# Optimization experiments

Measured on AMD Instinct MI355X. Metric: run time of the kernel, lower is better.

The kernel has to match this reference:

```python
import jax, jax.numpy as jnp
import numpy as np

RES = 0.1
TABLE = 2 ** 20
MOD_T = 201
HEADS = 8
M = 500_000
D = 120
PRIMES_NP = np.array([73856093, 19349669, 83492791], dtype=np.int64)
BMIN = np.array([-2.6, -8.1, 0.0], dtype=np.float32)
BMAX = np.array([4.6, 4.7, 3.1], dtype=np.float32)
CORNERS = [(0, 0, 0), (1, 0, 0), (0, 1, 0), (0, 0, 1), (1, 1, 0), (1, 0, 1), (0, 1, 1), (1, 1, 1)]


def _build_hash_table():
    # Mirror torch.arange / meshgrid voxel grid construction.
    xs = np.arange(BMIN[0], BMAX[0], RES, dtype=np.float32)
    ys = np.arange(BMIN[1], BMAX[1], RES, dtype=np.float32)
    zs = np.arange(BMIN[2], BMAX[2], RES, dtype=np.float32)
    gx, gy, gz = np.meshgrid(xs, ys, zs, indexing='ij')
    vox = np.stack([gx, gy, gz], axis=-1).reshape(-1, 3)
    grid = np.floor(vox / RES).astype(np.int64)
    h = np.remainder((grid * PRIMES_NP).sum(-1), TABLE)
    buf = np.full(TABLE, -1, dtype=np.int64)
    uh, first_idx = np.unique(h, return_index=True)
    buf[uh] = first_idx
    return buf, vox.shape[0]


def setup_inputs() -> dict:
    key = jax.random.key(0)
    ks = jax.random.split(key, 12)
    buf_np, total_voxels = _build_hash_table()
    u = jax.random.uniform(ks[0], (M, 3), dtype=jnp.float32)
    query_pts = jnp.asarray(BMIN) + u * jnp.asarray(BMAX - BMIN)
    query_times = jax.random.randint(ks[1], (M,), 0, 1000, dtype=jnp.int64)
    dynamic_features = jax.random.normal(ks[2], (total_voxels, D), dtype=jnp.float32) * 0.01
    time_embeddings = jax.random.normal(ks[3], (MOD_T, D), dtype=jnp.float32) * 0.01
    s = 1.0 / np.sqrt(D)
    Wq = jax.random.normal(ks[4], (D, D), dtype=jnp.float32) * s
    Wk = jax.random.normal(ks[5], (D, D), dtype=jnp.float32) * s
    Wv = jax.random.normal(ks[6], (D, D), dtype=jnp.float32) * s
    Wo = jax.random.normal(ks[7], (D, D), dtype=jnp.float32) * s
    bq = jnp.zeros((D,), jnp.float32)
    bk = jnp.zeros((D,), jnp.float32)
    bv = jnp.zeros((D,), jnp.float32)
    bo = jnp.zeros((D,), jnp.float32)
    return {
        'query_pts': query_pts, 'query_times': query_times,
        'dynamic_features': dynamic_features, 'time_embeddings': time_embeddings,
        'buffer_voxel_index': jnp.asarray(buf_np),
        'Wq': Wq, 'bq': bq, 'Wk': Wk, 'bk': bk, 'Wv': Wv, 'bv': bv, 'Wo': Wo, 'bo': bo,
    }


def _attn_fuse(feat, time_emb, Wq, bq, Wk, bk, Wv, bv, Wo, bo):
    # 2-token self-attention fusion: tokens = [voxel feature, time embedding]
    m, d = feat.shape
    dh = d // HEADS
    x = jnp.stack([feat, time_emb], axis=1)  # (M, 2, D)
    q = (x @ Wq + bq).reshape(m, 2, HEADS, dh)
    k = (x @ Wk + bk).reshape(m, 2, HEADS, dh)
    v = (x @ Wv + bv).reshape(m, 2, HEADS, dh)
    scores = jnp.einsum('mqhd,mkhd->mhqk', q, k) / jnp.sqrt(jnp.float32(dh))
    a = jax.nn.softmax(scores, axis=-1)
    o = jnp.einsum('mhqk,mkhd->mqhd', a, v).reshape(m, 2, d)
    o = o @ Wo + bo
    return o.mean(axis=1)  # (M, D)


def reference(query_pts, query_times, dynamic_features, time_embeddings,
              buffer_voxel_index, Wq, bq, Wk, bk, Wv, bv, Wo, bo):
    primes = jnp.asarray(PRIMES_NP)
    m = query_pts.shape[0]
    d = dynamic_features.shape[1]
    t_mod = jnp.remainder(query_times, MOD_T)

    gf = query_pts / RES
    gfl = jnp.floor(gf)
    frac = gf - gfl                      # (M, 3)
    base = gfl.astype(jnp.int64)         # (M, 3)

    accum = jnp.zeros((m, d), dtype=query_pts.dtype)
    for ox, oy, oz in CORNERS:           # fixed structural 8-corner loop
        cc = base + jnp.asarray([ox, oy, oz], dtype=jnp.int64)
        h = jnp.remainder((cc * primes).sum(-1), TABLE)
        vidx = buffer_voxel_index[h]
        valid = vidx >= 0
        wx = frac[:, 0] if ox else 1.0 - frac[:, 0]
        wy = frac[:, 1] if oy else 1.0 - frac[:, 1]
        wz = frac[:, 2] if oz else 1.0 - frac[:, 2]
        w = wx * wy * wz                 # (M,)
        f = dynamic_features[jnp.where(valid, vidx, 0)]
        accum = accum + jnp.where(valid[:, None], f * w[:, None], 0.0)

    time_emb = time_embeddings[t_mod]
    return _attn_fuse(accum, time_emb, Wq, bq, Wk, bk, Wv, bv, Wo, bo)
```

## Files before the change

### kernel.cpp

```cpp
#include <hip/hip_runtime.h>
#include <math.h>

#define M_D   120
#define MOD_T 201
#define TABLE_MASK 0xFFFFFu
#define INV_S 0.25819888974716115f

#define WS_TV  1608
#define WS_TQK 27336

typedef float    f32x4 __attribute__((ext_vector_type(4)));
typedef uint32_t u32x4 __attribute__((ext_vector_type(4)));
typedef __fp16   f16x2v __attribute__((ext_vector_type(2)));
typedef __fp16   f16x8 __attribute__((ext_vector_type(8)));

union PK2 { f16x2v h; uint32_t u; };
union BFrag { f16x8 v; f16x2v h2[4]; uint32_t u[4]; };

__global__ void precomp_time(const float* __restrict__ temb,
                             const float* __restrict__ Wq, const float* __restrict__ bq,
                             const float* __restrict__ Wk, const float* __restrict__ bk,
                             const float* __restrict__ Wv, const float* __restrict__ bv,
                             float* __restrict__ ws) {
  const int t = blockIdx.x, np = threadIdx.x;
  const int h = np >> 4, m = np & 15;
  const bool valid = (m < 15);
  const int col = h * 15 + m;
  __shared__ float lq[128], lk[128];
  float q = 0.f, k = 0.f, v = 0.f;
  if (valid) {
    q = bq[col]; k = bk[col]; v = bv[col];
    const float* te = temb + t * M_D;
    for (int i = 0; i < M_D; ++i) {
      float x = te[i];
      q = fmaf(x, Wq[i * M_D + col], q);
      k = fmaf(x, Wk[i * M_D + col], k);
      v = fmaf(x, Wv[i * M_D + col], v);
    }
  }
  lq[np] = q; lk[np] = k;
  ws[WS_TV + t * 128 + np] = v;
  PK2 pk; pk.h[0] = (__fp16)(q * INV_S); pk.h[1] = (__fp16)k;
  ((uint32_t*)ws)[WS_TQK + t * 128 + np] = pk.u;
  __syncthreads();
  if (np < 8) {
    float s = 0.f;
    #pragma unroll
    for (int mm = 0; mm < 15; ++mm) s += lq[np * 16 + mm] * lk[np * 16 + mm];
    ws[t * 8 + np] = s * INV_S;
  }
}

__launch_bounds__(512, 2)
__global__ void fused_main(const float* __restrict__ qpts, const int* __restrict__ qtimes,
                           const float* __restrict__ dyn,  const int* __restrict__ hbuf,
                           const float* __restrict__ Wq, const float* __restrict__ bq,
                           const float* __restrict__ Wk, const float* __restrict__ bk,
                           const float* __restrict__ Wv, const float* __restrict__ bv,
                           const float* __restrict__ Wo, const float* __restrict__ bo,
                           const float* __restrict__ ws, float* __restrict__ out, int M) {
  __shared__ __align__(16) uint32_t wlds[4 * 8192];

  const int tid = threadIdx.x;
  for (int idx = tid; idx < 32768; idx += 512) {
    const int mat = idx >> 13, r = idx & 8191;
    const int nt = r >> 10, kk = (r >> 8) & 3, l = (r >> 2) & 63, d = r & 3;
    const int mm = l & 15;
    const int i0 = kk * 32 + ((l >> 4) << 3) + 2 * d;
    float v0 = 0.f, v1 = 0.f;
    if (mat < 3) {
      const float* W = (mat == 0) ? Wq : (mat == 1) ? Wk : Wv;
      const float* b = (mat == 0) ? bq : (mat == 1) ? bk : bv;
      if (mm < 15) {
        const int col = nt * 15 + mm;
        const int ia = i0, ib = i0 + 1;
        v0 = (ia < 120) ? W[ia * M_D + col] : (ia == 120 ? b[col] : 0.f);
        v1 = (ib < 120) ? W[ib * M_D + col] : (ib == 120 ? b[col] : 0.f);
        if (mat == 0) { v0 *= INV_S; v1 *= INV_S; }
      }
    } else {
      const int n = nt * 16 + mm;
      if (n < M_D) {
        #pragma unroll
        for (int e = 0; e < 2; ++e) {
          const int ip = i0 + e;
          const int hi = ip >> 4, mi = ip & 15;
          float vv = 0.f;
          if (mi < 15) vv = Wo[(hi * 15 + mi) * M_D + n];
          else if (ip == 15) vv = bo[n];
          if (e == 0) v0 = vv; else v1 = vv;
        }
      }
    }
    PK2 pk; pk.h[0] = (__fp16)v0; pk.h[1] = (__fp16)v1;
    wlds[idx] = pk.u;
  }
  __syncthreads();

  const int l = tid & 63, wv = tid >> 6;
  const int g = l >> 4, pl = l & 15, c0 = g << 2;
  const float* S11 = ws;
  const float* TVt = ws + WS_TV;
  const uint32_t* TQK = (const uint32_t*)ws + WS_TQK;

  const int T = (M + 15) >> 4;
  for (int tile = blockIdx.x * 8 + wv; tile < T; tile += gridDim.x * 8) {
    const int pid = (tile << 4) + pl;
    const int p = (pid < M) ? pid : (M - 1);

    const float px = qpts[3 * p], py = qpts[3 * p + 1], pz = qpts[3 * p + 2];
    const int tm = qtimes[p] % MOD_T;
    const float gx = px / 0.1f, gy = py / 0.1f, gz = pz / 0.1f;
    const float fx = floorf(gx), fy = floorf(gy), fz = floorf(gz);
    const float rx = gx - fx, ry = gy - fy, rz = gz - fz;
    const int bx = (int)fx, by = (int)fy, bz = (int)fz;

    f32x4 accA[4] = {{0,0,0,0},{0,0,0,0},{0,0,0,0},{0,0,0,0}};
    f32x4 accB[4] = {{0,0,0,0},{0,0,0,0},{0,0,0,0},{0,0,0,0}};
    const int i0g = g * 8;
    #pragma unroll
    for (int c = 0; c < 8; ++c) {
      const int ox = c & 1, oy = (c >> 1) & 1, oz = c >> 2;
      const uint32_t hh = (uint32_t)(bx + ox) * 73856093u +
                          (uint32_t)(by + oy) * 19349669u +
                          (uint32_t)(bz + oz) * 83492791u;
      const int vc = hbuf[hh & TABLE_MASK];
      const float wc = (ox ? rx : 1.f - rx) * (oy ? ry : 1.f - ry) * (oz ? rz : 1.f - rz);
      if (vc >= 0) {
        const float* fr = dyn + (long)vc * M_D + i0g;
        #pragma unroll
        for (int kk = 0; kk < 4; ++kk) {
          if (kk < 3 || g < 3) {
            f32x4 lo4 = *(const f32x4*)(fr + kk * 32);
            f32x4 hi4 = *(const f32x4*)(fr + kk * 32 + 4);
            accA[kk] += lo4 * wc;
            accB[kk] += hi4 * wc;
          }
        }
      }
    }
    if (g == 3) accA[3][0] = 1.0f;

    BFrag bf[4];
    #pragma unroll
    for (int kk = 0; kk < 4; ++kk) {
      bf[kk].h2[0] = __builtin_amdgcn_cvt_pkrtz(accA[kk][0], accA[kk][1]);
      bf[kk].h2[1] = __builtin_amdgcn_cvt_pkrtz(accA[kk][2], accA[kk][3]);
      bf[kk].h2[2] = __builtin_amdgcn_cvt_pkrtz(accB[kk][0], accB[kk][1]);
      bf[kk].h2[3] = __builtin_amdgcn_cvt_pkrtz(accB[kk][2], accB[kk][3]);
    }

    f32x4 tvv[8]; u32x4 tqk[8]; float s11v[8];
    #pragma unroll
    for (int nt = 0; nt < 8; ++nt) {
      tvv[nt] = *(const f32x4*)(TVt + tm * 128 + nt * 16 + c0);
      tqk[nt] = *(const u32x4*)(TQK + tm * 128 + nt * 16 + c0);
      s11v[nt] = S11[tm * 8 + nt];
    }

    f32x4 aq[8], ak[8], av[8];
    #pragma unroll
    for (int nt = 0; nt < 8; ++nt) {
      f32x4 zq = {0,0,0,0}, zk = {0,0,0,0}, zv = {0,0,0,0};
      #pragma unroll
      for (int kk = 0; kk < 4; ++kk) {
        const int off = nt * 1024 + kk * 256 + l * 4;
        f16x8 a0 = *(const f16x8*)(wlds + off);
        f16x8 a1 = *(const f16x8*)(wlds + 8192 + off);
        f16x8 a2 = *(const f16x8*)(wlds + 16384 + off);
        zq = __builtin_amdgcn_mfma_f32_16x16x32_f16(a0, bf[kk].v, zq, 0, 0, 0);
        zk = __builtin_amdgcn_mfma_f32_16x16x32_f16(a1, bf[kk].v, zk, 0, 0, 0);
        zv = __builtin_amdgcn_mfma_f32_16x16x32_f16(a2, bf[kk].v, zv, 0, 0, 0);
      }
      aq[nt] = zq; ak[nt] = zk; av[nt] = zv;
    }

    float a_[8], b_[8];
    #pragma unroll
    for (int nt = 0; nt < 8; ++nt) {
      float s00 = 0.f, s01 = 0.f, s10 = 0.f;
      #pragma unroll
      for (int r = 0; r < 4; ++r) {
        const float qv = aq[nt][r], kv = ak[nt][r];
        PK2 tt; tt.u = tqk[nt][r];
        const float tqs = (float)tt.h[0], tk = (float)tt.h[1];
        s00 = fmaf(qv, kv, s00);
        s01 = fmaf(qv, tk, s01);
        s10 = fmaf(tqs, kv, s10);
      }
      s00 += __shfl_xor(s00, 16); s00 += __shfl_xor(s00, 32);
      s01 += __shfl_xor(s01, 16); s01 += __shfl_xor(s01, 32);
      s10 += __shfl_xor(s10, 16); s10 += __shfl_xor(s10, 32);
      const float s11 = s11v[nt];
      const float m0 = fmaxf(s00, s01), m1 = fmaxf(s10, s11);
      const float e00 = __expf(s00 - m0), e01 = __expf(s01 - m0);
      const float e10 = __expf(s10 - m1), e11 = __expf(s11 - m1);
      const float r0 = 1.f / (e00 + e01), r1 = 1.f / (e10 + e11);
      a_[nt] = 0.5f * (e00 * r0 + e10 * r1);
      b_[nt] = 0.5f * (e01 * r0 + e11 * r1);
    }

    uint32_t cdw[8][2];
    #pragma unroll
    for (int nt = 0; nt < 8; ++nt) {
      f32x4 cv;
      #pragma unroll
      for (int r = 0; r < 4; ++r) cv[r] = a_[nt] * av[nt][r] + b_[nt] * tvv[nt][r];
      if (nt == 0 && g == 3) cv[3] = 1.0f;
      PK2 p0, p1;
      p0.h = __builtin_amdgcn_cvt_pkrtz(cv[0], cv[1]);
      p1.h = __builtin_amdgcn_cvt_pkrtz(cv[2], cv[3]);
      cdw[nt][0] = p0.u; cdw[nt][1] = p1.u;
    }

    const int src0 = pl | ((g & 1) << 5);
    const int src1 = src0 + 16;
    const bool hsel = (g >= 2);
    BFrag bco[4];
    #pragma unroll
    for (int kk = 0; kk < 4; ++kk) {
      #pragma unroll
      for (int d = 0; d < 4; ++d) {
        const int s = (d >= 2) ? src1 : src0;
        const int vlo = __shfl((int)cdw[2 * kk][d & 1], s, 64);
        const int vhi = __shfl((int)cdw[2 * kk + 1][d & 1], s, 64);
        bco[kk].u[d] = hsel ? (uint32_t)vhi : (uint32_t)vlo;
      }
    }

    float* orow = out + (long)pid * M_D;
    #pragma unroll
    for (int nt = 0; nt < 8; ++nt) {
      f32x4 zo = {0,0,0,0};
      #pragma unroll
      for (int kk = 0; kk < 4; ++kk) {
        f16x8 a3 = *(const f16x8*)(wlds + 24576 + nt * 1024 + kk * 256 + l * 4);
        zo = __builtin_amdgcn_mfma_f32_16x16x32_f16(a3, bco[kk].v, zo, 0, 0, 0);
      }
      if (pid < M && (nt < 7 || g < 2))
        *(f32x4*)(orow + nt * 16 + c0) = zo;
    }
  }
}

extern "C" void kernel_launch(void* const* d_in, const int* in_sizes, int n_in,
                              void* d_out, int out_size, void* d_ws, size_t ws_size,
                              hipStream_t stream) {
  const float* qpts   = (const float*)d_in[0];
  const int*   qtimes = (const int*)d_in[1];
  const float* dyn    = (const float*)d_in[2];
  const float* temb   = (const float*)d_in[3];
  const int*   hbuf   = (const int*)d_in[4];
  const float* Wq = (const float*)d_in[5];
  const float* bq = (const float*)d_in[6];
  const float* Wk = (const float*)d_in[7];
  const float* bk = (const float*)d_in[8];
  const float* Wv = (const float*)d_in[9];
  const float* bv = (const float*)d_in[10];
  const float* Wo = (const float*)d_in[11];
  const float* bo = (const float*)d_in[12];
  float* out = (float*)d_out;
  float* ws  = (float*)d_ws;
  const int M = in_sizes[1];

  hipLaunchKernelGGL(precomp_time, dim3(MOD_T), dim3(128), 0, stream,
                     temb, Wq, bq, Wk, bk, Wv, bv, ws);
  hipLaunchKernelGGL(fused_main, dim3(256), dim3(512), 0, stream,
                     qpts, qtimes, dyn, hbuf, Wq, bq, Wk, bk, Wv, bv, Wo, bo, ws, out, M);
}
```

Measured before the change: 1.119 ms.

## Use 1024-thread blocks and make corner gathers branchless with kk-outer accumulation

Doubles the block size to 1024 threads (16 waves per block, one block per CU), so the 128 KB LDS weight copy is shared by twice as many waves and fewer blocks redo the LDS fill. The eight-corner gather is restructured: hash lookups first produce per-corner pointers and weights, with invalid corners redirected to row 0 at weight zero. The accumulation loop is then reordered so the k-slice is outermost, which needs only one pair of accumulators at a time and gives branchless loads the compiler can batch. The risks are higher register pressure under the 1024-thread launch bound and extra loads for invalid corners.

```diff
diff --git a/kernel.cpp b/kernel.cpp
--- a/kernel.cpp
+++ b/kernel.cpp
@@ -51,7 +51,7 @@
   }
 }
 
-__launch_bounds__(512, 2)
+__launch_bounds__(1024, 1)
 __global__ void fused_main(const float* __restrict__ qpts, const int* __restrict__ qtimes,
                            const float* __restrict__ dyn,  const int* __restrict__ hbuf,
                            const float* __restrict__ Wq, const float* __restrict__ bq,
@@ -62,7 +62,7 @@
   __shared__ __align__(16) uint32_t wlds[4 * 8192];
 
   const int tid = threadIdx.x;
-  for (int idx = tid; idx < 32768; idx += 512) {
+  for (int idx = tid; idx < 32768; idx += 1024) {
     const int mat = idx >> 13, r = idx & 8191;
     const int nt = r >> 10, kk = (r >> 8) & 3, l = (r >> 2) & 63, d = r & 3;
     const int mm = l & 15;
@@ -104,7 +104,7 @@
   const uint32_t* TQK = (const uint32_t*)ws + WS_TQK;
 
   const int T = (M + 15) >> 4;
-  for (int tile = blockIdx.x * 8 + wv; tile < T; tile += gridDim.x * 8) {
+  for (int tile = blockIdx.x * 16 + wv; tile < T; tile += gridDim.x * 16) {
     const int pid = (tile << 4) + pl;
     const int p = (pid < M) ? pid : (M - 1);
 
@@ -115,9 +115,9 @@
     const float rx = gx - fx, ry = gy - fy, rz = gz - fz;
     const int bx = (int)fx, by = (int)fy, bz = (int)fz;
 
-    f32x4 accA[4] = {{0,0,0,0},{0,0,0,0},{0,0,0,0},{0,0,0,0}};
-    f32x4 accB[4] = {{0,0,0,0},{0,0,0,0},{0,0,0,0},{0,0,0,0}};
     const int i0g = g * 8;
+    const float* frp[8];
+    float wcv[8];
     #pragma unroll
     for (int c = 0; c < 8; ++c) {
       const int ox = c & 1, oy = (c >> 1) & 1, oz = c >> 2;
@@ -126,28 +126,28 @@
                           (uint32_t)(bz + oz) * 83492791u;
       const int vc = hbuf[hh & TABLE_MASK];
       const float wc = (ox ? rx : 1.f - rx) * (oy ? ry : 1.f - ry) * (oz ? rz : 1.f - rz);
-      if (vc >= 0) {
-        const float* fr = dyn + (long)vc * M_D + i0g;
+      wcv[c] = (vc >= 0) ? wc : 0.f;
+      frp[c] = dyn + (long)((vc >= 0) ? vc : 0) * M_D + i0g;
+    }
+
+    BFrag bf[4];
+    #pragma unroll
+    for (int kk = 0; kk < 4; ++kk) {
+      f32x4 accA = {0, 0, 0, 0}, accB = {0, 0, 0, 0};
+      if (kk < 3 || g < 3) {
         #pragma unroll
-        for (int kk = 0; kk < 4; ++kk) {
-          if (kk < 3 || g < 3) {
-            f32x4 lo4 = *(const f32x4*)(fr + kk * 32);
-            f32x4 hi4 = *(const f32x4*)(fr + kk * 32 + 4);
-            accA[kk] += lo4 * wc;
-            accB[kk] += hi4 * wc;
-          }
+        for (int c = 0; c < 8; ++c) {
+          f32x4 lo4 = *(const f32x4*)(frp[c] + kk * 32);
+          f32x4 hi4 = *(const f32x4*)(frp[c] + kk * 32 + 4);
+          accA += lo4 * wcv[c];
+          accB += hi4 * wcv[c];
         }
       }
-    }
-    if (g == 3) accA[3][0] = 1.0f;
-
-    BFrag bf[4];
-    #pragma unroll
-    for (int kk = 0; kk < 4; ++kk) {
-      bf[kk].h2[0] = __builtin_amdgcn_cvt_pkrtz(accA[kk][0], accA[kk][1]);
-      bf[kk].h2[1] = __builtin_amdgcn_cvt_pkrtz(accA[kk][2], accA[kk][3]);
-      bf[kk].h2[2] = __builtin_amdgcn_cvt_pkrtz(accB[kk][0], accB[kk][1]);
-      bf[kk].h2[3] = __builtin_amdgcn_cvt_pkrtz(accB[kk][2], accB[kk][3]);
+      if (kk == 3 && g == 3) accA[0] = 1.0f;
+      bf[kk].h2[0] = __builtin_amdgcn_cvt_pkrtz(accA[0], accA[1]);
+      bf[kk].h2[1] = __builtin_amdgcn_cvt_pkrtz(accA[2], accA[3]);
+      bf[kk].h2[2] = __builtin_amdgcn_cvt_pkrtz(accB[0], accB[1]);
+      bf[kk].h2[3] = __builtin_amdgcn_cvt_pkrtz(accB[2], accB[3]);
     }
 
     f32x4 tvv[8]; u32x4 tqk[8]; float s11v[8];
@@ -265,6 +265,6 @@
 
   hipLaunchKernelGGL(precomp_time, dim3(MOD_T), dim3(128), 0, stream,
                      temb, Wq, bq, Wk, bk, Wv, bv, ws);
-  hipLaunchKernelGGL(fused_main, dim3(256), dim3(512), 0, stream,
+  hipLaunchKernelGGL(fused_main, dim3(256), dim3(1024), 0, stream,
                      qpts, qtimes, dyn, hbuf, Wq, bq, Wk, bk, Wv, bv, Wo, bo, ws, out, M);
 }
```

Result: slower. 1.904 ms (+70.2%).
